# Kernel optimization log

Measured on AMD Instinct MI355X. Metric: run time of the kernel, lower is better.

The kernel has to match this reference:

```python
import jax, jax.numpy as jnp
import numpy as np

B, Q, K, C, H, OUT = 4, 1024, 1024, 512, 8, 512
HD = C // H  # per-head key/value dim = 64


def setup_inputs() -> dict:
    key = jax.random.key(0)
    ks = jax.random.split(key, 9)
    glorot = lambda k, shape, fan: jax.random.uniform(k, shape, jnp.float32, -1.0, 1.0) * np.sqrt(3.0 / fan)
    fan_qk = (C + HD) / 2.0
    return {
        "q_data": jax.random.normal(ks[0], (B, Q, C), jnp.float32),
        "m_data": jax.random.normal(ks[1], (B, K, C), jnp.float32),
        "bias": jax.random.normal(ks[2], (B, 1, 1, K), jnp.float32),
        "nonbatched_bias": jax.random.normal(ks[3], (H, Q, K), jnp.float32),
        "query_w": glorot(ks[4], (C, H, HD), fan_qk),
        "key_w": glorot(ks[5], (C, H, HD), fan_qk),
        "value_w": glorot(ks[6], (C, H, HD), fan_qk),
        "gating_w": jnp.zeros((C, H, HD), jnp.float32),
        "gating_b": jnp.ones((H, HD), jnp.float32),
        "output_w": jnp.zeros((H, HD, OUT), jnp.float32),  # zero_init=True
        "output_b": jnp.zeros((OUT,), jnp.float32),
    }


def reference(q_data, m_data, bias, nonbatched_bias, query_w, key_w, value_w,
              gating_w, gating_b, output_w, output_b):
    key_dim = query_w.shape[-1]
    q = jnp.einsum('bqa,ahc->bqhc', q_data, query_w) * key_dim ** (-0.5)
    k = jnp.einsum('bka,ahc->bkhc', m_data, key_w)
    v = jnp.einsum('bka,ahc->bkhc', m_data, value_w)
    logits_update = jnp.einsum('bqhc,bkhc->bhqk', q, k)
    logits = logits_update + bias + nonbatched_bias[None]
    weights = jax.nn.softmax(logits, axis=-1)
    weighted_avg = jnp.einsum('bhqk,bkhc->bqhc', weights, v)
    gate = jax.nn.sigmoid(jnp.einsum('bqc,chv->bqhv', q_data, gating_w) + gating_b)
    weighted_avg = weighted_avg * gate
    output = jnp.einsum('bqhc,hco->bqo', weighted_avg, output_w) + output_b
    return (output, logits_update)
```

## Files before the change

### kernel.cpp

```cpp
#include <hip/hip_runtime.h>
#include <hip/hip_bf16.h>


typedef float f32x4 __attribute__((ext_vector_type(4)));
typedef __bf16 bf16x8 __attribute__((ext_vector_type(8)));
typedef __bf16 bf16x4 __attribute__((ext_vector_type(4)));

static __device__ __forceinline__ __bf16 f2bf(float x) {
    union { float f; unsigned int u; } c; c.f = x;
    unsigned int r = (c.u + 0x7fffu + ((c.u >> 16) & 1u)) >> 16;
    union { unsigned short s; __bf16 b; } o; o.s = (unsigned short)r;
    return o.b;
}

static __device__ __forceinline__ void async16(const void* g, void* l) {
    __builtin_amdgcn_global_load_lds(
        (const __attribute__((address_space(1))) void*)g,
        (__attribute__((address_space(3))) void*)l, 16, 0, 0);
}

__global__ __launch_bounds__(256) void cast_data(
    const float* __restrict__ qd, const float* __restrict__ md,
    __bf16* __restrict__ qdb, __bf16* __restrict__ mdb)
{
    const int i = blockIdx.x * 256 + threadIdx.x;
    const f32x4* q4 = (const f32x4*)qd;
    const f32x4* m4 = (const f32x4*)md;
    f32x4 a = q4[2 * i], b = q4[2 * i + 1];
    bf16x8 o;
#pragma unroll
    for (int j = 0; j < 4; j++) { o[j] = f2bf(a[j]); o[4 + j] = f2bf(b[j]); }
    *(bf16x8*)&qdb[i * 8] = o;
    a = m4[2 * i]; b = m4[2 * i + 1];
#pragma unroll
    for (int j = 0; j < 4; j++) { o[j] = f2bf(a[j]); o[4 + j] = f2bf(b[j]); }
    *(bf16x8*)&mdb[i * 8] = o;
}

__global__ __launch_bounds__(256) void transpose_cast(
    const float* __restrict__ qw, const float* __restrict__ kw,
    const float* __restrict__ vw, const float* __restrict__ gw,
    const float* __restrict__ ow,
    __bf16* __restrict__ qwt, __bf16* __restrict__ kwt,
    __bf16* __restrict__ vwt, __bf16* __restrict__ gwt,
    __bf16* __restrict__ owt)
{
    __shared__ float tile[64][65];
    const int z = blockIdx.z;
    const float* src = (z == 0) ? qw : (z == 1) ? kw : (z == 2) ? vw : (z == 3) ? gw : ow;
    __bf16* dst = (z == 0) ? qwt : (z == 1) ? kwt : (z == 2) ? vwt : (z == 3) ? gwt : owt;
    const float scale = (z == 0) ? 0.125f : 1.0f;
    const int a0 = blockIdx.x * 64, n0 = blockIdx.y * 64;
    const int t = threadIdx.x, tr = t >> 4, tc = (t & 15) * 4;
#pragma unroll
    for (int ii = 0; ii < 4; ii++) {
        f32x4 v = *(const f32x4*)&src[(a0 + tr + 16 * ii) * 512 + n0 + tc];
#pragma unroll
        for (int j = 0; j < 4; j++) tile[tr + 16 * ii][tc + j] = v[j] * scale;
    }
    __syncthreads();
#pragma unroll
    for (int ii = 0; ii < 4; ii++) {
        const int nr = tr + 16 * ii;
        bf16x4 o;
#pragma unroll
        for (int j = 0; j < 4; j++) o[j] = f2bf(tile[tc + j][nr]);
        *(bf16x4*)&dst[(n0 + nr) * 512 + a0 + tc] = o;
    }
}

static __device__ __forceinline__ void gemm_core64(
    const __bf16* __restrict__ A, const __bf16* __restrict__ Bt,
    __bf16* As, __bf16* Bs, int m0, int n0, int t, f32x4 acc[4])
{
    const int w = t >> 6, quad = (t >> 4) & 3, col = t & 15;
    const int sr = t >> 2, sc = (t & 3) * 8;
    for (int kk = 0; kk < 512; kk += 32) {
        __syncthreads();
        async16(&A[(m0 + sr) * 512 + kk + sc], &As[w * 512]);
        async16(&Bt[(n0 + sr) * 512 + kk + sc], &Bs[w * 512]);
        __syncthreads();
        bf16x8 af = *(const bf16x8*)&As[(w * 16 + col) * 32 + quad * 8];
#pragma unroll
        for (int ns = 0; ns < 4; ns++) {
            bf16x8 bfr = *(const bf16x8*)&Bs[(ns * 16 + col) * 32 + quad * 8];
            acc[ns] = __builtin_amdgcn_mfma_f32_16x16x32_bf16(af, bfr, acc[ns], 0, 0, 0);
        }
    }
}

static __device__ __forceinline__ void gemm_core128(
    const __bf16* __restrict__ A, const __bf16* __restrict__ Bt,
    __bf16* As, __bf16* Bs, int m0, int n0, int t, f32x4 acc[4][4])
{
    const int w = t >> 6, quad = (t >> 4) & 3, col = t & 15;
    const int wr = (w >> 1) * 64, wc = (w & 1) * 64;
    const int sr = t >> 2, sc = (t & 3) * 8;
    for (int kk = 0; kk < 512; kk += 32) {
        __syncthreads();
        async16(&A[(m0 + sr) * 512 + kk + sc], &As[w * 512]);
        async16(&A[(m0 + 64 + sr) * 512 + kk + sc], &As[2048 + w * 512]);
        async16(&Bt[(n0 + sr) * 512 + kk + sc], &Bs[w * 512]);
        async16(&Bt[(n0 + 64 + sr) * 512 + kk + sc], &Bs[2048 + w * 512]);
        __syncthreads();
        bf16x8 af[4], bfr[4];
#pragma unroll
        for (int i = 0; i < 4; i++)
            af[i] = *(const bf16x8*)&As[(wr + i * 16 + col) * 32 + quad * 8];
#pragma unroll
        for (int i = 0; i < 4; i++)
            bfr[i] = *(const bf16x8*)&Bs[(wc + i * 16 + col) * 32 + quad * 8];
#pragma unroll
        for (int mi = 0; mi < 4; mi++)
#pragma unroll
            for (int ni = 0; ni < 4; ni++)
                acc[mi][ni] = __builtin_amdgcn_mfma_f32_16x16x32_bf16(
                    af[mi], bfr[ni], acc[mi][ni], 0, 0, 0);
    }
}

__global__ __launch_bounds__(256) void proj_gemm(
    const __bf16* __restrict__ qdb, const __bf16* __restrict__ mdb,
    const __bf16* __restrict__ qwt, const __bf16* __restrict__ kwt,
    const __bf16* __restrict__ vwt, const __bf16* __restrict__ gwt,
    __bf16* __restrict__ qbuf, __bf16* __restrict__ kbuf,
    __bf16* __restrict__ vt, __bf16* __restrict__ gate,
    const float* __restrict__ gb)
{
    __shared__ __attribute__((aligned(16))) __bf16 As[4096];
    __shared__ __attribute__((aligned(16))) __bf16 Bs[4096];
    const int z = blockIdx.z;
    const __bf16* A = (z == 0 || z == 3) ? qdb : mdb;
    const __bf16* Bt = (z == 0) ? qwt : (z == 1) ? kwt : (z == 2) ? vwt : gwt;
    const int m0 = blockIdx.x * 128, n0 = blockIdx.y * 128;
    f32x4 acc[4][4];
#pragma unroll
    for (int i = 0; i < 4; i++)
#pragma unroll
        for (int j = 0; j < 4; j++) acc[i][j] = (f32x4){0.f, 0.f, 0.f, 0.f};
    gemm_core128(A, Bt, As, Bs, m0, n0, threadIdx.x, acc);

    const int t = threadIdx.x, w = t >> 6, quad = (t >> 4) & 3, col = t & 15;
    const int wr = (w >> 1) * 64, wc = (w & 1) * 64;
#pragma unroll
    for (int mi = 0; mi < 4; mi++) {
#pragma unroll
        for (int ni = 0; ni < 4; ni++) {
            const int ncol = n0 + wc + ni * 16 + col;
#pragma unroll
            for (int r = 0; r < 4; r++) {
                const int m = m0 + wr + mi * 16 + quad * 4 + r;
                const float v = acc[mi][ni][r];
                if (z <= 1) {
                    int b = m >> 10, pos = m & 1023, hh = ncol >> 6, c = ncol & 63;
                    __bf16* o = z ? kbuf : qbuf;
                    o[(((b * 8 + hh) * 1024 + pos) << 6) + c] = f2bf(v);
                } else if (z == 2) {
                    int b = m >> 10, pos = m & 1023, hh = ncol >> 6, c = ncol & 63;
                    vt[((((b * 8 + hh) << 6) + c) << 10) + pos] = f2bf(v);
                } else {
                    float g = 1.0f / (1.0f + __expf(-(v + gb[ncol])));
                    gate[m * 512 + ncol] = f2bf(g);
                }
            }
        }
    }
}

__global__ __launch_bounds__(256) void out_gemm(
    const __bf16* __restrict__ A, const __bf16* __restrict__ Bt,
    float* __restrict__ outp, const float* __restrict__ bvec)
{
    __shared__ __attribute__((aligned(16))) __bf16 As[2048];
    __shared__ __attribute__((aligned(16))) __bf16 Bs[2048];
    const int m0 = blockIdx.x * 64, n0 = blockIdx.y * 64;
    f32x4 acc[4];
#pragma unroll
    for (int i = 0; i < 4; i++) acc[i] = (f32x4){0.f, 0.f, 0.f, 0.f};
    gemm_core64(A, Bt, As, Bs, m0, n0, threadIdx.x, acc);

    const int t = threadIdx.x, w = t >> 6, quad = (t >> 4) & 3, col = t & 15;
    const int mrow0 = m0 + w * 16 + quad * 4;
#pragma unroll
    for (int ns = 0; ns < 4; ns++) {
        const int ncol = n0 + ns * 16 + col;
#pragma unroll
        for (int r = 0; r < 4; r++)
            outp[(mrow0 + r) * 512 + ncol] = acc[ns][r] + bvec[ncol];
    }
}

__global__ __launch_bounds__(256) void attn_kernel(
    const __bf16* __restrict__ qb, const __bf16* __restrict__ kb,
    const __bf16* __restrict__ vt, const float* __restrict__ bias,
    const float* __restrict__ nb, const __bf16* __restrict__ gate,
    float* __restrict__ logits_out, __bf16* __restrict__ wout)
{
    __shared__ __attribute__((aligned(16))) __bf16 ks[2][4096];
    __shared__ __attribute__((aligned(16))) __bf16 vs[2][4096];
    __shared__ __attribute__((aligned(16))) __bf16 ps[4][1152];
    __shared__ __attribute__((aligned(16))) float bs[1024];

    const int bh = blockIdx.y, b = bh >> 3, h = bh & 7;
    const int q0 = blockIdx.x * 64;
    const int t = threadIdx.x, lane = t & 63, w = t >> 6;
    const int quad = lane >> 4, col = lane & 15;

    const __bf16* kg = kb + bh * 65536;
    const __bf16* vg = vt + bh * 65536;
    float* lg = logits_out + (size_t)(bh * 1024 + q0) * 1024;
    const float* nbg = nb + (size_t)(h * 1024 + q0) * 1024;
    const float* biasg = bias + b * 1024;

    const int r0 = t >> 3, c0 = t & 7;
    const int sw = ((c0 ^ (r0 & 7)) << 3);

    async16(&kg[r0 * 64 + sw], &ks[0][w * 512]);
    async16(&kg[(r0 + 32) * 64 + sw], &ks[0][2048 + w * 512]);
    async16(&vg[r0 * 1024 + sw], &vs[0][w * 512]);
    async16(&vg[(r0 + 32) * 1024 + sw], &vs[0][2048 + w * 512]);
    async16(&biasg[lane * 4], (char*)bs + w * 1024);

    const __bf16* qrow = qb + (size_t)(bh * 1024 + q0 + w * 16 + col) * 64;
    const bf16x8 af0 = *(const bf16x8*)&qrow[quad * 8];
    const bf16x8 af1 = *(const bf16x8*)&qrow[32 + quad * 8];

    const float* nbrow = nbg + (w * 16 + col) * 1024 + quad * 4;
    f32x4 nbr4[4];
#pragma unroll
    for (int ns = 0; ns < 4; ns++) nbr4[ns] = *(const f32x4*)&nbrow[ns * 16];

    f32x4 o_acc[4];
#pragma unroll
    for (int i = 0; i < 4; i++) o_acc[i] = (f32x4){0.f, 0.f, 0.f, 0.f};
    float lsum = 0.f;

    __bf16* pw = ps[w];
    const int sw0 = ((quad ^ (col & 7)) << 3);
    const int sw1 = (((quad + 4) ^ (col & 7)) << 3);

    __syncthreads();

    for (int kbi = 0; kbi < 16; kbi++) {
        const int cur = kbi & 1;
        if (kbi < 15) {
            const int nx = cur ^ 1;
            const __bf16* kgn = kg + (kbi + 1) * 4096;
            const __bf16* vgn = vg + (kbi + 1) * 64;
            async16(&kgn[r0 * 64 + sw], &ks[nx][w * 512]);
            async16(&kgn[(r0 + 32) * 64 + sw], &ks[nx][2048 + w * 512]);
            async16(&vgn[r0 * 1024 + sw], &vs[nx][w * 512]);
            async16(&vgn[(r0 + 32) * 1024 + sw], &vs[nx][2048 + w * 512]);
        }
        __builtin_amdgcn_sched_barrier(0);
        f32x4 nbrn4[4];
        if (kbi < 15) {
#pragma unroll
            for (int ns = 0; ns < 4; ns++)
                nbrn4[ns] = *(const f32x4*)&nbrow[(kbi + 1) * 64 + ns * 16];
        }
        const __bf16* kc = ks[cur];
        const __bf16* vc = vs[cur];

        f32x4 s[4];
#pragma unroll
        for (int i = 0; i < 4; i++) s[i] = (f32x4){0.f, 0.f, 0.f, 0.f};
        __builtin_amdgcn_s_setprio(1);
#pragma unroll
        for (int ns = 0; ns < 4; ns++) {
            bf16x8 b0 = *(const bf16x8*)&kc[(ns * 16 + col) * 64 + sw0];
            s[ns] = __builtin_amdgcn_mfma_f32_16x16x32_bf16(b0, af0, s[ns], 0, 0, 0);
            bf16x8 b1 = *(const bf16x8*)&kc[(ns * 16 + col) * 64 + sw1];
            s[ns] = __builtin_amdgcn_mfma_f32_16x16x32_bf16(b1, af1, s[ns], 0, 0, 0);
        }
        __builtin_amdgcn_s_setprio(0);

        float* lrow = lg + (w * 16 + col) * 1024 + kbi * 64;
#pragma unroll
        for (int ns = 0; ns < 4; ns++) {
            f32x4 raw = s[ns];
            __builtin_nontemporal_store(raw, (f32x4*)&lrow[ns * 16 + quad * 4]);
            f32x4 bv = *(const f32x4*)&bs[kbi * 64 + ns * 16 + quad * 4];
            bf16x4 pk;
#pragma unroll
            for (int r = 0; r < 4; r++) {
                float p = __expf(raw[r] + bv[r] + nbr4[ns][r]);
                lsum += p;
                pk[r] = f2bf(p);
            }
            *(bf16x4*)&pw[col * 72 + ns * 16 + quad * 4] = pk;
        }

        bf16x8 pf0 = *(const bf16x8*)&pw[col * 72 + quad * 8];
        bf16x8 pf1 = *(const bf16x8*)&pw[col * 72 + 32 + quad * 8];
        __builtin_amdgcn_s_setprio(1);
#pragma unroll
        for (int ns = 0; ns < 4; ns++) {
            bf16x8 v0 = *(const bf16x8*)&vc[(ns * 16 + col) * 64 + sw0];
            o_acc[ns] = __builtin_amdgcn_mfma_f32_16x16x32_bf16(pf0, v0, o_acc[ns], 0, 0, 0);
            bf16x8 v1 = *(const bf16x8*)&vc[(ns * 16 + col) * 64 + sw1];
            o_acc[ns] = __builtin_amdgcn_mfma_f32_16x16x32_bf16(pf1, v1, o_acc[ns], 0, 0, 0);
        }
        __builtin_amdgcn_s_setprio(0);

        if (kbi < 15) {
#pragma unroll
            for (int ns = 0; ns < 4; ns++) nbr4[ns] = nbrn4[ns];
            asm volatile("s_waitcnt lgkmcnt(0)" ::: "memory");
            asm volatile("s_waitcnt vmcnt(8)" ::: "memory");
            __builtin_amdgcn_sched_barrier(0);
            __builtin_amdgcn_s_barrier();
            __builtin_amdgcn_sched_barrier(0);
        }
    }

    lsum += __shfl_xor(lsum, 16, 64);
    lsum += __shfl_xor(lsum, 32, 64);
    float inv = 1.0f / lsum;
    float invr[4];
#pragma unroll
    for (int r = 0; r < 4; r++) invr[r] = __shfl(inv, quad * 4 + r, 64);

#pragma unroll
    for (int ns = 0; ns < 4; ns++) {
        const int c = ns * 16 + col;
#pragma unroll
        for (int r = 0; r < 4; r++) {
            const int pos = q0 + w * 16 + quad * 4 + r;
            float ov = o_acc[ns][r] * invr[r];
            float gv = (float)gate[(b * 1024 + pos) * 512 + h * 64 + c];
            wout[(b * 1024 + pos) * 512 + h * 64 + c] = f2bf(ov * gv);
        }
    }
}

extern "C" void kernel_launch(void* const* d_in, const int* in_sizes, int n_in,
                              void* d_out, int out_size, void* d_ws, size_t ws_size,
                              hipStream_t stream) {
    (void)in_sizes; (void)n_in; (void)out_size; (void)ws_size;
    const float* q_data   = (const float*)d_in[0];
    const float* m_data   = (const float*)d_in[1];
    const float* bias     = (const float*)d_in[2];
    const float* nbb      = (const float*)d_in[3];
    const float* query_w  = (const float*)d_in[4];
    const float* key_w    = (const float*)d_in[5];
    const float* value_w  = (const float*)d_in[6];
    const float* gating_w = (const float*)d_in[7];
    const float* gating_b = (const float*)d_in[8];
    const float* output_w = (const float*)d_in[9];
    const float* output_b = (const float*)d_in[10];

    char* ws = (char*)d_ws;
    __bf16* qd_b  = (__bf16*)(ws + 0);
    __bf16* md_b  = (__bf16*)(ws + 4194304);
    __bf16* qw_t  = (__bf16*)(ws + 8388608);
    __bf16* kw_t  = (__bf16*)(ws + 8912896);
    __bf16* vw_t  = (__bf16*)(ws + 9437184);
    __bf16* gw_t  = (__bf16*)(ws + 9961472);
    __bf16* ow_t  = (__bf16*)(ws + 10485760);
    __bf16* q_buf = (__bf16*)(ws + 11010048);
    __bf16* k_buf = (__bf16*)(ws + 15204352);
    __bf16* v_t   = (__bf16*)(ws + 19398656);
    __bf16* gate  = (__bf16*)(ws + 23592960);
    __bf16* wavg  = (__bf16*)(ws + 0);

    float* outp = (float*)d_out;
    float* logits = outp + (4 * 1024 * 512);

    cast_data<<<dim3(1024), dim3(256), 0, stream>>>(q_data, m_data, qd_b, md_b);
    transpose_cast<<<dim3(8, 8, 5), dim3(256), 0, stream>>>(
        query_w, key_w, value_w, gating_w, output_w, qw_t, kw_t, vw_t, gw_t, ow_t);
    proj_gemm<<<dim3(32, 4, 4), dim3(256), 0, stream>>>(
        qd_b, md_b, qw_t, kw_t, vw_t, gw_t, q_buf, k_buf, v_t, gate, gating_b);
    attn_kernel<<<dim3(16, 32), dim3(256), 0, stream>>>(
        q_buf, k_buf, v_t, bias, nbb, gate, logits, wavg);
    out_gemm<<<dim3(64, 8), dim3(256), 0, stream>>>(wavg, ow_t, outp, output_b);
}
```

Before: 268.1 us.

## Split attention key blocks across wave pairs and halve query tile per block

The attention kernel now handles 32 queries per block instead of 64. Waves are split into two query strips and two key halves, and the partial PV accumulators and row sums are reduced through shared memory at the end. The grid doubles to 1024 blocks and launch bounds request 4 blocks per CU, aiming for more occupancy and parallelism. In exchange, each block reloads the same K/V tiles for half as many queries (twice the K/V traffic overall), and the end now carries an extra reduction and barrier. Bias is read straight from global into registers instead of being staged in LDS.

After: 277.9 us. 3.7% more time.

```diff
diff --git a/kernel.cpp b/kernel.cpp
--- a/kernel.cpp
+++ b/kernel.cpp
@@ -190,7 +190,7 @@
     }
 }
 
-__global__ __launch_bounds__(256) void attn_kernel(
+__global__ __launch_bounds__(256, 4) void attn_kernel(
     const __bf16* __restrict__ qb, const __bf16* __restrict__ kb,
     const __bf16* __restrict__ vt, const float* __restrict__ bias,
     const float* __restrict__ nb, const __bf16* __restrict__ gate,
@@ -198,13 +198,14 @@
 {
     __shared__ __attribute__((aligned(16))) __bf16 ks[2][4096];
     __shared__ __attribute__((aligned(16))) __bf16 vs[2][4096];
-    __shared__ __attribute__((aligned(16))) __bf16 ps[4][1152];
-    __shared__ __attribute__((aligned(16))) float bs[1024];
+    __shared__ __attribute__((aligned(16))) float scratch[2048];
 
     const int bh = blockIdx.y, b = bh >> 3, h = bh & 7;
-    const int q0 = blockIdx.x * 64;
+    const int q0 = blockIdx.x * 32;
     const int t = threadIdx.x, lane = t & 63, w = t >> 6;
     const int quad = lane >> 4, col = lane & 15;
+    const int s = w & 1;
+    const int kh = w >> 1;
 
     const __bf16* kg = kb + bh * 65536;
     const __bf16* vg = vt + bh * 65536;
@@ -219,25 +220,29 @@
     async16(&kg[(r0 + 32) * 64 + sw], &ks[0][2048 + w * 512]);
     async16(&vg[r0 * 1024 + sw], &vs[0][w * 512]);
     async16(&vg[(r0 + 32) * 1024 + sw], &vs[0][2048 + w * 512]);
-    async16(&biasg[lane * 4], (char*)bs + w * 1024);
-
-    const __bf16* qrow = qb + (size_t)(bh * 1024 + q0 + w * 16 + col) * 64;
+
+    const __bf16* qrow = qb + (size_t)(bh * 1024 + q0 + s * 16 + col) * 64;
     const bf16x8 af0 = *(const bf16x8*)&qrow[quad * 8];
     const bf16x8 af1 = *(const bf16x8*)&qrow[32 + quad * 8];
 
-    const float* nbrow = nbg + (w * 16 + col) * 1024 + quad * 4;
-    f32x4 nbr4[4];
-#pragma unroll
-    for (int ns = 0; ns < 4; ns++) nbr4[ns] = *(const f32x4*)&nbrow[ns * 16];
+    const float* nbrow = nbg + (s * 16 + col) * 1024 + kh * 32 + quad * 4;
+    const float* brow  = biasg + kh * 32 + quad * 4;
+    f32x4 nbr4[2], bv4[2];
+#pragma unroll
+    for (int ns = 0; ns < 2; ns++) {
+        nbr4[ns] = *(const f32x4*)&nbrow[ns * 16];
+        bv4[ns]  = *(const f32x4*)&brow[ns * 16];
+    }
 
     f32x4 o_acc[4];
 #pragma unroll
     for (int i = 0; i < 4; i++) o_acc[i] = (f32x4){0.f, 0.f, 0.f, 0.f};
     float lsum = 0.f;
 
-    __bf16* pw = ps[w];
+    __bf16* pss = (__bf16*)scratch + s * 1152;
     const int sw0 = ((quad ^ (col & 7)) << 3);
     const int sw1 = (((quad + 4) ^ (col & 7)) << 3);
+    const int swp = (((kh * 4 + quad) ^ (col & 7)) << 3);
 
     __syncthreads();
 
@@ -253,83 +258,98 @@
             async16(&vgn[(r0 + 32) * 1024 + sw], &vs[nx][2048 + w * 512]);
         }
         __builtin_amdgcn_sched_barrier(0);
-        f32x4 nbrn4[4];
+        f32x4 nbrn4[2], bvn4[2];
         if (kbi < 15) {
 #pragma unroll
-            for (int ns = 0; ns < 4; ns++)
+            for (int ns = 0; ns < 2; ns++) {
                 nbrn4[ns] = *(const f32x4*)&nbrow[(kbi + 1) * 64 + ns * 16];
+                bvn4[ns]  = *(const f32x4*)&brow[(kbi + 1) * 64 + ns * 16];
+            }
         }
         const __bf16* kc = ks[cur];
         const __bf16* vc = vs[cur];
 
-        f32x4 s[4];
-#pragma unroll
-        for (int i = 0; i < 4; i++) s[i] = (f32x4){0.f, 0.f, 0.f, 0.f};
+        f32x4 sacc[2];
+#pragma unroll
+        for (int i = 0; i < 2; i++) sacc[i] = (f32x4){0.f, 0.f, 0.f, 0.f};
         __builtin_amdgcn_s_setprio(1);
 #pragma unroll
-        for (int ns = 0; ns < 4; ns++) {
-            bf16x8 b0 = *(const bf16x8*)&kc[(ns * 16 + col) * 64 + sw0];
-            s[ns] = __builtin_amdgcn_mfma_f32_16x16x32_bf16(b0, af0, s[ns], 0, 0, 0);
-            bf16x8 b1 = *(const bf16x8*)&kc[(ns * 16 + col) * 64 + sw1];
-            s[ns] = __builtin_amdgcn_mfma_f32_16x16x32_bf16(b1, af1, s[ns], 0, 0, 0);
+        for (int ns = 0; ns < 2; ns++) {
+            bf16x8 b0 = *(const bf16x8*)&kc[(kh * 32 + ns * 16 + col) * 64 + sw0];
+            sacc[ns] = __builtin_amdgcn_mfma_f32_16x16x32_bf16(b0, af0, sacc[ns], 0, 0, 0);
+            bf16x8 b1 = *(const bf16x8*)&kc[(kh * 32 + ns * 16 + col) * 64 + sw1];
+            sacc[ns] = __builtin_amdgcn_mfma_f32_16x16x32_bf16(b1, af1, sacc[ns], 0, 0, 0);
         }
         __builtin_amdgcn_s_setprio(0);
 
-        float* lrow = lg + (w * 16 + col) * 1024 + kbi * 64;
-#pragma unroll
-        for (int ns = 0; ns < 4; ns++) {
-            f32x4 raw = s[ns];
+        float* lrow = lg + (s * 16 + col) * 1024 + kbi * 64 + kh * 32;
+#pragma unroll
+        for (int ns = 0; ns < 2; ns++) {
+            f32x4 raw = sacc[ns];
             __builtin_nontemporal_store(raw, (f32x4*)&lrow[ns * 16 + quad * 4]);
-            f32x4 bv = *(const f32x4*)&bs[kbi * 64 + ns * 16 + quad * 4];
             bf16x4 pk;
 #pragma unroll
             for (int r = 0; r < 4; r++) {
-                float p = __expf(raw[r] + bv[r] + nbr4[ns][r]);
+                float p = __expf(raw[r] + bv4[ns][r] + nbr4[ns][r]);
                 lsum += p;
                 pk[r] = f2bf(p);
             }
-            *(bf16x4*)&pw[col * 72 + ns * 16 + quad * 4] = pk;
-        }
-
-        bf16x8 pf0 = *(const bf16x8*)&pw[col * 72 + quad * 8];
-        bf16x8 pf1 = *(const bf16x8*)&pw[col * 72 + 32 + quad * 8];
+            *(bf16x4*)&pss[col * 72 + kh * 32 + ns * 16 + quad * 4] = pk;
+        }
+
+        bf16x8 pf = *(const bf16x8*)&pss[col * 72 + kh * 32 + quad * 8];
         __builtin_amdgcn_s_setprio(1);
 #pragma unroll
         for (int ns = 0; ns < 4; ns++) {
-            bf16x8 v0 = *(const bf16x8*)&vc[(ns * 16 + col) * 64 + sw0];
-            o_acc[ns] = __builtin_amdgcn_mfma_f32_16x16x32_bf16(pf0, v0, o_acc[ns], 0, 0, 0);
-            bf16x8 v1 = *(const bf16x8*)&vc[(ns * 16 + col) * 64 + sw1];
-            o_acc[ns] = __builtin_amdgcn_mfma_f32_16x16x32_bf16(pf1, v1, o_acc[ns], 0, 0, 0);
+            bf16x8 v0 = *(const bf16x8*)&vc[(ns * 16 + col) * 64 + swp];
+            o_acc[ns] = __builtin_amdgcn_mfma_f32_16x16x32_bf16(pf, v0, o_acc[ns], 0, 0, 0);
         }
         __builtin_amdgcn_s_setprio(0);
 
         if (kbi < 15) {
 #pragma unroll
-            for (int ns = 0; ns < 4; ns++) nbr4[ns] = nbrn4[ns];
+            for (int ns = 0; ns < 2; ns++) { nbr4[ns] = nbrn4[ns]; bv4[ns] = bvn4[ns]; }
             asm volatile("s_waitcnt lgkmcnt(0)" ::: "memory");
-            asm volatile("s_waitcnt vmcnt(8)" ::: "memory");
+            asm volatile("s_waitcnt vmcnt(6)" ::: "memory");
             __builtin_amdgcn_sched_barrier(0);
             __builtin_amdgcn_s_barrier();
             __builtin_amdgcn_sched_barrier(0);
         }
     }
 
+    __syncthreads();
+    float* ored = scratch;
+    float* lred = (float*)ks;
+
     lsum += __shfl_xor(lsum, 16, 64);
     lsum += __shfl_xor(lsum, 32, 64);
-    float inv = 1.0f / lsum;
-    float invr[4];
-#pragma unroll
-    for (int r = 0; r < 4; r++) invr[r] = __shfl(inv, quad * 4 + r, 64);
-
-#pragma unroll
-    for (int ns = 0; ns < 4; ns++) {
-        const int c = ns * 16 + col;
-#pragma unroll
-        for (int r = 0; r < 4; r++) {
-            const int pos = q0 + w * 16 + quad * 4 + r;
-            float ov = o_acc[ns][r] * invr[r];
-            float gv = (float)gate[(b * 1024 + pos) * 512 + h * 64 + c];
-            wout[(b * 1024 + pos) * 512 + h * 64 + c] = f2bf(ov * gv);
+
+    if (kh == 1) {
+#pragma unroll
+        for (int ns = 0; ns < 4; ns++)
+#pragma unroll
+            for (int r = 0; r < 4; r++)
+                ored[s * 1024 + (quad * 4 + r) * 64 + ns * 16 + col] = o_acc[ns][r];
+        if (quad == 0) lred[s * 16 + col] = lsum;
+    }
+    __syncthreads();
+
+    if (kh == 0) {
+        const float inv = 1.0f / (lsum + lred[s * 16 + col]);
+        float invr[4];
+#pragma unroll
+        for (int r = 0; r < 4; r++) invr[r] = __shfl(inv, quad * 4 + r, 64);
+#pragma unroll
+        for (int ns = 0; ns < 4; ns++) {
+            const int c = ns * 16 + col;
+#pragma unroll
+            for (int r = 0; r < 4; r++) {
+                const int pos = q0 + s * 16 + quad * 4 + r;
+                float ov = (o_acc[ns][r] +
+                            ored[s * 1024 + (quad * 4 + r) * 64 + ns * 16 + col]) * invr[r];
+                float gv = (float)gate[(b * 1024 + pos) * 512 + h * 64 + c];
+                wout[(b * 1024 + pos) * 512 + h * 64 + c] = f2bf(ov * gv);
+            }
         }
     }
 }
@@ -372,7 +392,7 @@
         query_w, key_w, value_w, gating_w, output_w, qw_t, kw_t, vw_t, gw_t, ow_t);
     proj_gemm<<<dim3(32, 4, 4), dim3(256), 0, stream>>>(
         qd_b, md_b, qw_t, kw_t, vw_t, gw_t, q_buf, k_buf, v_t, gate, gating_b);
-    attn_kernel<<<dim3(16, 32), dim3(256), 0, stream>>>(
+    attn_kernel<<<dim3(32, 32), dim3(256), 0, stream>>>(
         q_buf, k_buf, v_t, bias, nbb, gate, logits, wavg);
     out_gemm<<<dim3(64, 8), dim3(256), 0, stream>>>(wavg, ow_t, outp, output_b);
 }
```

## Split attention over key range across two waves with direct register K/V loads

Applied to the files above, without the earlier changes.

The attention kernel moves from 64-query blocks of four waves sharing LDS-staged K/V tiles to 16-query blocks of two waves. Each wave handles half of the key range and loads K, V, the bias and the non-batched bias straight from global memory into registers, double-buffered across steps. The partial outputs and softmax sums are combined through LDS at the end, and the block index is remapped so neighbouring blocks spread across heads and batches. This removes LDS staging and per-step barriers and raises the block count, but each K/V tile is now read from global memory by four times as many blocks, relying on cache reuse.

Result: slower. 327.7 us (+22.2%).

```diff
diff --git a/kernel.cpp b/kernel.cpp
--- a/kernel.cpp
+++ b/kernel.cpp
@@ -190,146 +190,125 @@
     }
 }
 
-__global__ __launch_bounds__(256) void attn_kernel(
+__global__ __launch_bounds__(128) void attn_kernel(
     const __bf16* __restrict__ qb, const __bf16* __restrict__ kb,
     const __bf16* __restrict__ vt, const float* __restrict__ bias,
     const float* __restrict__ nb, const __bf16* __restrict__ gate,
     float* __restrict__ logits_out, __bf16* __restrict__ wout)
 {
-    __shared__ __attribute__((aligned(16))) __bf16 ks[2][4096];
-    __shared__ __attribute__((aligned(16))) __bf16 vs[2][4096];
-    __shared__ __attribute__((aligned(16))) __bf16 ps[4][1152];
-    __shared__ __attribute__((aligned(16))) float bs[1024];
-
-    const int bh = blockIdx.y, b = bh >> 3, h = bh & 7;
-    const int q0 = blockIdx.x * 64;
+    __shared__ __attribute__((aligned(16))) __bf16 psc[2][576];
+    __shared__ __attribute__((aligned(16))) float ored[1024];
+    __shared__ float lred[16];
+
+    const int f = blockIdx.y * 64 + blockIdx.x;
+    const int sfl = (f & 7) * 256 + (f >> 3);
+    const int qx = sfl & 63, bh = sfl >> 6;
+    const int b = bh >> 3, h = bh & 7;
+    const int q0 = qx * 16;
     const int t = threadIdx.x, lane = t & 63, w = t >> 6;
     const int quad = lane >> 4, col = lane & 15;
+    const int kb0 = w * 512;
 
     const __bf16* kg = kb + bh * 65536;
     const __bf16* vg = vt + bh * 65536;
     float* lg = logits_out + (size_t)(bh * 1024 + q0) * 1024;
-    const float* nbg = nb + (size_t)(h * 1024 + q0) * 1024;
-    const float* biasg = bias + b * 1024;
-
-    const int r0 = t >> 3, c0 = t & 7;
-    const int sw = ((c0 ^ (r0 & 7)) << 3);
-
-    async16(&kg[r0 * 64 + sw], &ks[0][w * 512]);
-    async16(&kg[(r0 + 32) * 64 + sw], &ks[0][2048 + w * 512]);
-    async16(&vg[r0 * 1024 + sw], &vs[0][w * 512]);
-    async16(&vg[(r0 + 32) * 1024 + sw], &vs[0][2048 + w * 512]);
-    async16(&biasg[lane * 4], (char*)bs + w * 1024);
-
-    const __bf16* qrow = qb + (size_t)(bh * 1024 + q0 + w * 16 + col) * 64;
+    const float* nbr = nb + (size_t)(h * 1024 + q0 + col) * 1024;
+    const float* bg = bias + b * 1024;
+
+    const __bf16* qrow = qb + (size_t)(bh * 1024 + q0 + col) * 64;
     const bf16x8 af0 = *(const bf16x8*)&qrow[quad * 8];
     const bf16x8 af1 = *(const bf16x8*)&qrow[32 + quad * 8];
 
-    const float* nbrow = nbg + (w * 16 + col) * 1024 + quad * 4;
-    f32x4 nbr4[4];
-#pragma unroll
-    for (int ns = 0; ns < 4; ns++) nbr4[ns] = *(const f32x4*)&nbrow[ns * 16];
-
     f32x4 o_acc[4];
 #pragma unroll
     for (int i = 0; i < 4; i++) o_acc[i] = (f32x4){0.f, 0.f, 0.f, 0.f};
     float lsum = 0.f;
-
-    __bf16* pw = ps[w];
-    const int sw0 = ((quad ^ (col & 7)) << 3);
-    const int sw1 = (((quad + 4) ^ (col & 7)) << 3);
-
-    __syncthreads();
-
-    for (int kbi = 0; kbi < 16; kbi++) {
-        const int cur = kbi & 1;
-        if (kbi < 15) {
-            const int nx = cur ^ 1;
-            const __bf16* kgn = kg + (kbi + 1) * 4096;
-            const __bf16* vgn = vg + (kbi + 1) * 64;
-            async16(&kgn[r0 * 64 + sw], &ks[nx][w * 512]);
-            async16(&kgn[(r0 + 32) * 64 + sw], &ks[nx][2048 + w * 512]);
-            async16(&vgn[r0 * 1024 + sw], &vs[nx][w * 512]);
-            async16(&vgn[(r0 + 32) * 1024 + sw], &vs[nx][2048 + w * 512]);
-        }
-        __builtin_amdgcn_sched_barrier(0);
-        f32x4 nbrn4[4];
-        if (kbi < 15) {
-#pragma unroll
-            for (int ns = 0; ns < 4; ns++)
-                nbrn4[ns] = *(const f32x4*)&nbrow[(kbi + 1) * 64 + ns * 16];
-        }
-        const __bf16* kc = ks[cur];
-        const __bf16* vc = vs[cur];
-
-        f32x4 s[4];
-#pragma unroll
-        for (int i = 0; i < 4; i++) s[i] = (f32x4){0.f, 0.f, 0.f, 0.f};
+    __bf16* pw = psc[w];
+
+    auto LOADT = [&](int kt, bf16x8 kA[2][2], bf16x8 vB[4], f32x4 nbv[2]) {
+        const int kr = kb0 + kt * 32;
+#pragma unroll
+        for (int ns = 0; ns < 2; ns++) {
+#pragma unroll
+            for (int hf = 0; hf < 2; hf++)
+                kA[ns][hf] = *(const bf16x8*)&kg[(kr + ns * 16 + col) * 64 + hf * 32 + quad * 8];
+            nbv[ns] = *(const f32x4*)&nbr[kr + ns * 16 + quad * 4];
+        }
+#pragma unroll
+        for (int ns = 0; ns < 4; ns++)
+            vB[ns] = *(const bf16x8*)&vg[(ns * 16 + col) * 1024 + kr + quad * 8];
+    };
+
+    auto STEP = [&](int kt, bf16x8 kA[2][2], bf16x8 vB[4], f32x4 nbv[2]) {
+        const int kr = kb0 + kt * 32;
+        float* lrow = lg + col * 1024 + kr;
         __builtin_amdgcn_s_setprio(1);
-#pragma unroll
-        for (int ns = 0; ns < 4; ns++) {
-            bf16x8 b0 = *(const bf16x8*)&kc[(ns * 16 + col) * 64 + sw0];
-            s[ns] = __builtin_amdgcn_mfma_f32_16x16x32_bf16(b0, af0, s[ns], 0, 0, 0);
-            bf16x8 b1 = *(const bf16x8*)&kc[(ns * 16 + col) * 64 + sw1];
-            s[ns] = __builtin_amdgcn_mfma_f32_16x16x32_bf16(b1, af1, s[ns], 0, 0, 0);
-        }
+        f32x4 s0 = (f32x4){0.f, 0.f, 0.f, 0.f}, s1 = s0;
+        s0 = __builtin_amdgcn_mfma_f32_16x16x32_bf16(kA[0][0], af0, s0, 0, 0, 0);
+        s0 = __builtin_amdgcn_mfma_f32_16x16x32_bf16(kA[0][1], af1, s0, 0, 0, 0);
+        s1 = __builtin_amdgcn_mfma_f32_16x16x32_bf16(kA[1][0], af0, s1, 0, 0, 0);
+        s1 = __builtin_amdgcn_mfma_f32_16x16x32_bf16(kA[1][1], af1, s1, 0, 0, 0);
         __builtin_amdgcn_s_setprio(0);
-
-        float* lrow = lg + (w * 16 + col) * 1024 + kbi * 64;
-#pragma unroll
-        for (int ns = 0; ns < 4; ns++) {
-            f32x4 raw = s[ns];
+#pragma unroll
+        for (int ns = 0; ns < 2; ns++) {
+            f32x4 raw = ns ? s1 : s0;
             __builtin_nontemporal_store(raw, (f32x4*)&lrow[ns * 16 + quad * 4]);
-            f32x4 bv = *(const f32x4*)&bs[kbi * 64 + ns * 16 + quad * 4];
+            f32x4 bv = *(const f32x4*)&bg[kr + ns * 16 + quad * 4];
             bf16x4 pk;
 #pragma unroll
             for (int r = 0; r < 4; r++) {
-                float p = __expf(raw[r] + bv[r] + nbr4[ns][r]);
+                float p = __expf(raw[r] + bv[r] + nbv[ns][r]);
                 lsum += p;
                 pk[r] = f2bf(p);
             }
-            *(bf16x4*)&pw[col * 72 + ns * 16 + quad * 4] = pk;
-        }
-
-        bf16x8 pf0 = *(const bf16x8*)&pw[col * 72 + quad * 8];
-        bf16x8 pf1 = *(const bf16x8*)&pw[col * 72 + 32 + quad * 8];
+            *(bf16x4*)&pw[col * 36 + ns * 16 + quad * 4] = pk;
+        }
+        bf16x8 pf = *(const bf16x8*)&pw[col * 36 + quad * 8];
         __builtin_amdgcn_s_setprio(1);
 #pragma unroll
-        for (int ns = 0; ns < 4; ns++) {
-            bf16x8 v0 = *(const bf16x8*)&vc[(ns * 16 + col) * 64 + sw0];
-            o_acc[ns] = __builtin_amdgcn_mfma_f32_16x16x32_bf16(pf0, v0, o_acc[ns], 0, 0, 0);
-            bf16x8 v1 = *(const bf16x8*)&vc[(ns * 16 + col) * 64 + sw1];
-            o_acc[ns] = __builtin_amdgcn_mfma_f32_16x16x32_bf16(pf1, v1, o_acc[ns], 0, 0, 0);
-        }
+        for (int ns = 0; ns < 4; ns++)
+            o_acc[ns] = __builtin_amdgcn_mfma_f32_16x16x32_bf16(pf, vB[ns], o_acc[ns], 0, 0, 0);
         __builtin_amdgcn_s_setprio(0);
-
-        if (kbi < 15) {
-#pragma unroll
-            for (int ns = 0; ns < 4; ns++) nbr4[ns] = nbrn4[ns];
-            asm volatile("s_waitcnt lgkmcnt(0)" ::: "memory");
-            asm volatile("s_waitcnt vmcnt(8)" ::: "memory");
-            __builtin_amdgcn_sched_barrier(0);
-            __builtin_amdgcn_s_barrier();
-            __builtin_amdgcn_sched_barrier(0);
-        }
+    };
+
+    bf16x8 kAa[2][2], vBa[4], kAb[2][2], vBb[4];
+    f32x4 nba[2], nbb2[2];
+    LOADT(0, kAa, vBa, nba);
+#pragma unroll
+    for (int kt = 0; kt < 16; kt += 2) {
+        LOADT(kt + 1, kAb, vBb, nbb2);
+        STEP(kt, kAa, vBa, nba);
+        if (kt + 2 < 16) LOADT(kt + 2, kAa, vBa, nba);
+        STEP(kt + 1, kAb, vBb, nbb2);
     }
 
     lsum += __shfl_xor(lsum, 16, 64);
     lsum += __shfl_xor(lsum, 32, 64);
-    float inv = 1.0f / lsum;
-    float invr[4];
-#pragma unroll
-    for (int r = 0; r < 4; r++) invr[r] = __shfl(inv, quad * 4 + r, 64);
-
-#pragma unroll
-    for (int ns = 0; ns < 4; ns++) {
-        const int c = ns * 16 + col;
-#pragma unroll
-        for (int r = 0; r < 4; r++) {
-            const int pos = q0 + w * 16 + quad * 4 + r;
-            float ov = o_acc[ns][r] * invr[r];
-            float gv = (float)gate[(b * 1024 + pos) * 512 + h * 64 + c];
-            wout[(b * 1024 + pos) * 512 + h * 64 + c] = f2bf(ov * gv);
+
+    if (w == 1) {
+#pragma unroll
+        for (int ns = 0; ns < 4; ns++)
+#pragma unroll
+            for (int r = 0; r < 4; r++)
+                ored[(quad * 4 + r) * 64 + ns * 16 + col] = o_acc[ns][r];
+        if (quad == 0) lred[col] = lsum;
+    }
+    __syncthreads();
+    if (w == 0) {
+        const float inv = 1.0f / (lsum + lred[col]);
+        float invr[4];
+#pragma unroll
+        for (int r = 0; r < 4; r++) invr[r] = __shfl(inv, quad * 4 + r, 64);
+#pragma unroll
+        for (int ns = 0; ns < 4; ns++) {
+            const int c = ns * 16 + col;
+#pragma unroll
+            for (int r = 0; r < 4; r++) {
+                const int pos = q0 + quad * 4 + r;
+                float ov = (o_acc[ns][r] + ored[(quad * 4 + r) * 64 + c]) * invr[r];
+                float gv = (float)gate[(b * 1024 + pos) * 512 + h * 64 + c];
+                wout[(b * 1024 + pos) * 512 + h * 64 + c] = f2bf(ov * gv);
+            }
         }
     }
 }
@@ -372,7 +351,7 @@
         query_w, key_w, value_w, gating_w, output_w, qw_t, kw_t, vw_t, gw_t, ow_t);
     proj_gemm<<<dim3(32, 4, 4), dim3(256), 0, stream>>>(
         qd_b, md_b, qw_t, kw_t, vw_t, gw_t, q_buf, k_buf, v_t, gate, gating_b);
-    attn_kernel<<<dim3(16, 32), dim3(256), 0, stream>>>(
+    attn_kernel<<<dim3(64, 32), dim3(128), 0, stream>>>(
         q_buf, k_buf, v_t, bias, nbb, gate, logits, wavg);
     out_gemm<<<dim3(64, 8), dim3(256), 0, stream>>>(wavg, ow_t, outp, output_b);
 }
```

## Split fused attention into QK logits kernel and separate softmax-PV kernel

Applied to the files above, without the earlier changes.

Splits the fused attention kernel into a QK GEMM that only writes logits, and a separate PV kernel. The PV kernel re-reads the logits from global memory, applies the bias and exp, and multiplies by V with a split-K over two waves, reduced through shared memory. The intent is more parallelism and simpler per-kernel pipelines. The cost is an extra full read of the fp32 logits tensor and an additional launch.

New measurement: 334.1 us. +24.6%, slower.

```diff
diff --git a/kernel.cpp b/kernel.cpp
--- a/kernel.cpp
+++ b/kernel.cpp
@@ -190,78 +190,40 @@
     }
 }
 
-__global__ __launch_bounds__(256) void attn_kernel(
+__global__ __launch_bounds__(256) void qk_gemm(
     const __bf16* __restrict__ qb, const __bf16* __restrict__ kb,
-    const __bf16* __restrict__ vt, const float* __restrict__ bias,
-    const float* __restrict__ nb, const __bf16* __restrict__ gate,
-    float* __restrict__ logits_out, __bf16* __restrict__ wout)
+    float* __restrict__ logits_out)
 {
     __shared__ __attribute__((aligned(16))) __bf16 ks[2][4096];
-    __shared__ __attribute__((aligned(16))) __bf16 vs[2][4096];
-    __shared__ __attribute__((aligned(16))) __bf16 ps[4][1152];
-    __shared__ __attribute__((aligned(16))) float bs[1024];
-
-    const int bh = blockIdx.y, b = bh >> 3, h = bh & 7;
+    const int bh = blockIdx.y;
     const int q0 = blockIdx.x * 64;
     const int t = threadIdx.x, lane = t & 63, w = t >> 6;
     const int quad = lane >> 4, col = lane & 15;
 
     const __bf16* kg = kb + bh * 65536;
-    const __bf16* vg = vt + bh * 65536;
     float* lg = logits_out + (size_t)(bh * 1024 + q0) * 1024;
-    const float* nbg = nb + (size_t)(h * 1024 + q0) * 1024;
-    const float* biasg = bias + b * 1024;
 
     const int r0 = t >> 3, c0 = t & 7;
     const int sw = ((c0 ^ (r0 & 7)) << 3);
-
     async16(&kg[r0 * 64 + sw], &ks[0][w * 512]);
     async16(&kg[(r0 + 32) * 64 + sw], &ks[0][2048 + w * 512]);
-    async16(&vg[r0 * 1024 + sw], &vs[0][w * 512]);
-    async16(&vg[(r0 + 32) * 1024 + sw], &vs[0][2048 + w * 512]);
-    async16(&biasg[lane * 4], (char*)bs + w * 1024);
 
     const __bf16* qrow = qb + (size_t)(bh * 1024 + q0 + w * 16 + col) * 64;
     const bf16x8 af0 = *(const bf16x8*)&qrow[quad * 8];
     const bf16x8 af1 = *(const bf16x8*)&qrow[32 + quad * 8];
-
-    const float* nbrow = nbg + (w * 16 + col) * 1024 + quad * 4;
-    f32x4 nbr4[4];
-#pragma unroll
-    for (int ns = 0; ns < 4; ns++) nbr4[ns] = *(const f32x4*)&nbrow[ns * 16];
-
-    f32x4 o_acc[4];
-#pragma unroll
-    for (int i = 0; i < 4; i++) o_acc[i] = (f32x4){0.f, 0.f, 0.f, 0.f};
-    float lsum = 0.f;
-
-    __bf16* pw = ps[w];
     const int sw0 = ((quad ^ (col & 7)) << 3);
     const int sw1 = (((quad + 4) ^ (col & 7)) << 3);
 
     __syncthreads();
-
     for (int kbi = 0; kbi < 16; kbi++) {
         const int cur = kbi & 1;
         if (kbi < 15) {
-            const int nx = cur ^ 1;
             const __bf16* kgn = kg + (kbi + 1) * 4096;
-            const __bf16* vgn = vg + (kbi + 1) * 64;
-            async16(&kgn[r0 * 64 + sw], &ks[nx][w * 512]);
-            async16(&kgn[(r0 + 32) * 64 + sw], &ks[nx][2048 + w * 512]);
-            async16(&vgn[r0 * 1024 + sw], &vs[nx][w * 512]);
-            async16(&vgn[(r0 + 32) * 1024 + sw], &vs[nx][2048 + w * 512]);
+            async16(&kgn[r0 * 64 + sw], &ks[cur ^ 1][w * 512]);
+            async16(&kgn[(r0 + 32) * 64 + sw], &ks[cur ^ 1][2048 + w * 512]);
         }
         __builtin_amdgcn_sched_barrier(0);
-        f32x4 nbrn4[4];
-        if (kbi < 15) {
-#pragma unroll
-            for (int ns = 0; ns < 4; ns++)
-                nbrn4[ns] = *(const f32x4*)&nbrow[(kbi + 1) * 64 + ns * 16];
-        }
         const __bf16* kc = ks[cur];
-        const __bf16* vc = vs[cur];
-
         f32x4 s[4];
 #pragma unroll
         for (int i = 0; i < 4; i++) s[i] = (f32x4){0.f, 0.f, 0.f, 0.f};
@@ -274,62 +236,143 @@
             s[ns] = __builtin_amdgcn_mfma_f32_16x16x32_bf16(b1, af1, s[ns], 0, 0, 0);
         }
         __builtin_amdgcn_s_setprio(0);
-
         float* lrow = lg + (w * 16 + col) * 1024 + kbi * 64;
 #pragma unroll
-        for (int ns = 0; ns < 4; ns++) {
-            f32x4 raw = s[ns];
-            __builtin_nontemporal_store(raw, (f32x4*)&lrow[ns * 16 + quad * 4]);
-            f32x4 bv = *(const f32x4*)&bs[kbi * 64 + ns * 16 + quad * 4];
-            bf16x4 pk;
-#pragma unroll
-            for (int r = 0; r < 4; r++) {
-                float p = __expf(raw[r] + bv[r] + nbr4[ns][r]);
-                lsum += p;
-                pk[r] = f2bf(p);
-            }
-            *(bf16x4*)&pw[col * 72 + ns * 16 + quad * 4] = pk;
-        }
-
-        bf16x8 pf0 = *(const bf16x8*)&pw[col * 72 + quad * 8];
-        bf16x8 pf1 = *(const bf16x8*)&pw[col * 72 + 32 + quad * 8];
-        __builtin_amdgcn_s_setprio(1);
-#pragma unroll
-        for (int ns = 0; ns < 4; ns++) {
-            bf16x8 v0 = *(const bf16x8*)&vc[(ns * 16 + col) * 64 + sw0];
-            o_acc[ns] = __builtin_amdgcn_mfma_f32_16x16x32_bf16(pf0, v0, o_acc[ns], 0, 0, 0);
-            bf16x8 v1 = *(const bf16x8*)&vc[(ns * 16 + col) * 64 + sw1];
-            o_acc[ns] = __builtin_amdgcn_mfma_f32_16x16x32_bf16(pf1, v1, o_acc[ns], 0, 0, 0);
-        }
-        __builtin_amdgcn_s_setprio(0);
-
+        for (int ns = 0; ns < 4; ns++)
+            __builtin_nontemporal_store(s[ns], (f32x4*)&lrow[ns * 16 + quad * 4]);
         if (kbi < 15) {
-#pragma unroll
-            for (int ns = 0; ns < 4; ns++) nbr4[ns] = nbrn4[ns];
             asm volatile("s_waitcnt lgkmcnt(0)" ::: "memory");
-            asm volatile("s_waitcnt vmcnt(8)" ::: "memory");
+            asm volatile("s_waitcnt vmcnt(4)" ::: "memory");
             __builtin_amdgcn_sched_barrier(0);
             __builtin_amdgcn_s_barrier();
             __builtin_amdgcn_sched_barrier(0);
         }
     }
-
+}
+
+__global__ __launch_bounds__(128, 4) void pv_kernel(
+    const float* __restrict__ logits, const float* __restrict__ bias,
+    const float* __restrict__ nb, const __bf16* __restrict__ vt,
+    const __bf16* __restrict__ gate, __bf16* __restrict__ wout)
+{
+    __shared__ __attribute__((aligned(16))) __bf16 vsl[2][2][2048];
+    __shared__ __attribute__((aligned(16))) float bs[1024];
+
+    const int bh = blockIdx.y, b = bh >> 3, h = bh & 7;
+    const int q0 = blockIdx.x * 16;
+    const int t = threadIdx.x, lane = t & 63, w = t >> 6;
+    const int quad = lane >> 4, col = lane & 15;
+    const int kh = w;
+
+    const __bf16* vg = vt + bh * 65536;
+    const float* lgr = logits + (size_t)(bh * 1024 + q0 + col) * 1024 + kh * 512;
+    const float* nbp = nb + (size_t)(h * 1024 + q0 + col) * 1024 + kh * 512;
+    const float* bg = bias + b * 1024;
+
+    async16(&bg[w * 256 + lane * 4], (char*)bs + w * 1024);
+    async16(&bg[512 + w * 256 + lane * 4], (char*)bs + 2048 + w * 1024);
+
+    f32x4 o_acc[4];
+#pragma unroll
+    for (int i = 0; i < 4; i++) o_acc[i] = (f32x4){0.f, 0.f, 0.f, 0.f};
+    float lsum = 0.f;
+
+    auto PFV = [&](int kt) {
+        const __bf16* src = vg + kh * 512 + kt * 32;
+        __bf16* dst = &vsl[w][kt & 1][0];
+#pragma unroll
+        for (int c = 0; c < 4; c++) {
+            const int row = c * 16 + (lane >> 2);
+            const int slot = lane & 3;
+            async16(&src[row * 1024 + ((slot ^ (row & 3)) << 3)], dst + c * 512);
+        }
+    };
+    auto LOADL = [&](int kt, f32x4 L[2], f32x4 N[2]) {
+        const float* lp = lgr + kt * 32;
+        const float* np = nbp + kt * 32;
+        L[0] = *(const f32x4*)&lp[quad * 8];
+        L[1] = *(const f32x4*)&lp[quad * 8 + 4];
+        N[0] = *(const f32x4*)&np[quad * 8];
+        N[1] = *(const f32x4*)&np[quad * 8 + 4];
+    };
+    auto STEP = [&](int kt, const f32x4 L[2], const f32x4 N[2]) {
+        const f32x4 bv0 = *(const f32x4*)&bs[kh * 512 + kt * 32 + quad * 8];
+        const f32x4 bv1 = *(const f32x4*)&bs[kh * 512 + kt * 32 + quad * 8 + 4];
+        bf16x8 pf;
+#pragma unroll
+        for (int j = 0; j < 4; j++) {
+            float p = __expf(L[0][j] + bv0[j] + N[0][j]);
+            lsum += p; pf[j] = f2bf(p);
+        }
+#pragma unroll
+        for (int j = 0; j < 4; j++) {
+            float p = __expf(L[1][j] + bv1[j] + N[1][j]);
+            lsum += p; pf[4 + j] = f2bf(p);
+        }
+        const __bf16* vc = &vsl[w][kt & 1][0];
+        __builtin_amdgcn_s_setprio(1);
+#pragma unroll
+        for (int ns = 0; ns < 4; ns++) {
+            const int row = ns * 16 + col;
+            bf16x8 vb = *(const bf16x8*)&vc[row * 32 + ((quad ^ (row & 3)) << 3)];
+            o_acc[ns] = __builtin_amdgcn_mfma_f32_16x16x32_bf16(pf, vb, o_acc[ns], 0, 0, 0);
+        }
+        __builtin_amdgcn_s_setprio(0);
+    };
+
+    __syncthreads();
+
+    f32x4 La[2], Na[2], Lb[2], Nb[2];
+    PFV(0); LOADL(0, La, Na);
+#pragma unroll
+    for (int kt = 0; kt < 16; kt += 2) {
+        PFV(kt + 1); LOADL(kt + 1, Lb, Nb);
+        asm volatile("s_waitcnt vmcnt(8)" ::: "memory");
+        STEP(kt, La, Na);
+        asm volatile("s_waitcnt lgkmcnt(0)" ::: "memory");
+        __builtin_amdgcn_sched_barrier(0);
+        if (kt + 2 < 16) {
+            PFV(kt + 2); LOADL(kt + 2, La, Na);
+            asm volatile("s_waitcnt vmcnt(8)" ::: "memory");
+        } else {
+            asm volatile("s_waitcnt vmcnt(4)" ::: "memory");
+        }
+        STEP(kt + 1, Lb, Nb);
+        if (kt + 2 < 16) {
+            asm volatile("s_waitcnt lgkmcnt(0)" ::: "memory");
+            __builtin_amdgcn_sched_barrier(0);
+        }
+    }
+
+    __syncthreads();
+    float* ored = (float*)vsl;
+    float* lred = ored + 1024;
     lsum += __shfl_xor(lsum, 16, 64);
     lsum += __shfl_xor(lsum, 32, 64);
-    float inv = 1.0f / lsum;
-    float invr[4];
-#pragma unroll
-    for (int r = 0; r < 4; r++) invr[r] = __shfl(inv, quad * 4 + r, 64);
-
-#pragma unroll
-    for (int ns = 0; ns < 4; ns++) {
-        const int c = ns * 16 + col;
-#pragma unroll
-        for (int r = 0; r < 4; r++) {
-            const int pos = q0 + w * 16 + quad * 4 + r;
-            float ov = o_acc[ns][r] * invr[r];
-            float gv = (float)gate[(b * 1024 + pos) * 512 + h * 64 + c];
-            wout[(b * 1024 + pos) * 512 + h * 64 + c] = f2bf(ov * gv);
+    if (w == 1) {
+#pragma unroll
+        for (int ns = 0; ns < 4; ns++)
+#pragma unroll
+            for (int r = 0; r < 4; r++)
+                ored[(quad * 4 + r) * 64 + ns * 16 + col] = o_acc[ns][r];
+        if (lane < 16) lred[lane] = lsum;
+    }
+    __syncthreads();
+    if (w == 0) {
+        const float inv = 1.0f / (lsum + lred[col]);
+        float invr[4];
+#pragma unroll
+        for (int r = 0; r < 4; r++) invr[r] = __shfl(inv, quad * 4 + r, 64);
+#pragma unroll
+        for (int ns = 0; ns < 4; ns++) {
+            const int c = ns * 16 + col;
+#pragma unroll
+            for (int r = 0; r < 4; r++) {
+                const int pos = q0 + quad * 4 + r;
+                float ov = (o_acc[ns][r] + ored[(quad * 4 + r) * 64 + c]) * invr[r];
+                float gv = (float)gate[(b * 1024 + pos) * 512 + h * 64 + c];
+                wout[(b * 1024 + pos) * 512 + h * 64 + c] = f2bf(ov * gv);
+            }
         }
     }
 }
@@ -372,7 +415,8 @@
         query_w, key_w, value_w, gating_w, output_w, qw_t, kw_t, vw_t, gw_t, ow_t);
     proj_gemm<<<dim3(32, 4, 4), dim3(256), 0, stream>>>(
         qd_b, md_b, qw_t, kw_t, vw_t, gw_t, q_buf, k_buf, v_t, gate, gating_b);
-    attn_kernel<<<dim3(16, 32), dim3(256), 0, stream>>>(
-        q_buf, k_buf, v_t, bias, nbb, gate, logits, wavg);
+    qk_gemm<<<dim3(16, 32), dim3(256), 0, stream>>>(q_buf, k_buf, logits);
+    pv_kernel<<<dim3(64, 32), dim3(128), 0, stream>>>(
+        logits, bias, nbb, v_t, gate, wavg);
     out_gemm<<<dim3(64, 8), dim3(256), 0, stream>>>(wavg, ow_t, outp, output_b);
 }
```
